# Kernel optimization log

Hardware: AMD Instinct MI355X
Metric: run time of the kernel (lower is better)

The kernel has to match this reference:

```python
import jax, jax.numpy as jnp
import numpy as np

B, C, H, W = 512, 1, 280, 280
KS, S, P_PAD, F = 28, 28, 0, 16
HS = (H - KS + 2 * P_PAD) // S + 1  # 10
WS = (W - KS + 2 * P_PAD) // S + 1  # 10
P = HS * WS                          # 100 patches
OUT = 10


def setup_inputs() -> dict:
    key = jax.random.key(0)
    k1, k2, k3, k4, k5 = jax.random.split(key, 5)
    x = jax.random.normal(k1, (B, C, H, W), dtype=jnp.float32)
    weight = jax.random.normal(k2, (P * F, C, KS, KS), dtype=jnp.float32) * 0.05
    bias = jax.random.normal(k3, (P * F, C), dtype=jnp.float32) * 0.05
    dec_w = jax.random.normal(k4, (OUT, P * F * C), dtype=jnp.float32) * 0.05
    dec_b = jax.random.normal(k5, (OUT,), dtype=jnp.float32) * 0.05
    return {"x": x, "weight": weight, "bias": bias, "dec_w": dec_w, "dec_b": dec_b}


def _extract_patches(x):
    # x: (B, C, H+2p, W+2p) -> (B, P, C, KS, KS), patch order: row-major over (hs, ws)
    rows = jnp.arange(HS)[:, None] * S + jnp.arange(KS)[None, :]  # (HS, KS)
    cols = jnp.arange(WS)[:, None] * S + jnp.arange(KS)[None, :]  # (WS, KS)
    p = x[:, :, rows, :]            # (B, C, HS, KS, W)
    p = p[:, :, :, :, cols]         # (B, C, HS, KS, WS, KS)
    p = p.transpose(0, 2, 4, 1, 3, 5)  # (B, HS, WS, C, KS, KS)
    return p.reshape(B, P, C, KS, KS)


def reference(x, weight, bias, dec_w, dec_b):
    xp = jnp.pad(x, ((0, 0), (0, 0), (P_PAD, P_PAD), (P_PAD, P_PAD)))
    patches = _extract_patches(xp)                       # (B, P, C, KS, KS)
    # torch: x.repeat(1, f, ...) tiles patches f times; weight flat index i -> (f_idx, p_idx)
    w = weight.reshape(F, P, C, KS, KS)
    y = jnp.einsum('bpckl,fpckl->bfpc', patches, w)      # (B, F, P, C)
    y = y + bias.reshape(F, P, C)
    y = jax.nn.relu(y)
    y = y.reshape(B, F * P * C)
    return y @ dec_w.T + dec_b
```

## Files before the change

### kernel.cpp

```cpp
#include <hip/hip_runtime.h>
#include <stdint.h>

#define BATCH 512
#define HWIMG 78400
#define WROW  280
#define KSZ   28
#define PNUM  100
#define FNUM  16
#define ONUM  10

#define BT    64
#define CH    7
#define XF4   (BT * 28)
#define WF4   (FNUM * 28)

typedef __attribute__((address_space(1))) const void cg_void;
typedef __attribute__((address_space(3))) void lds_void;

__global__ __launch_bounds__(256) void init_out(const float* __restrict__ dec_b,
                                                float* __restrict__ out) {
    int i = blockIdx.x * 256 + threadIdx.x;
    if (i < BATCH * ONUM) out[i] = dec_b[i % ONUM];
}

__global__ __launch_bounds__(256) void lcn_fused(
    const float* __restrict__ x,
    const float* __restrict__ weight,
    const float* __restrict__ bias,
    const float* __restrict__ dec_w,
    float* __restrict__ out)
{
    __shared__ float4 lx[2][XF4];
    __shared__ float4 lw[2][WF4];

    const int t  = threadIdx.x;
    const int kg = t & 7;
    const int fg = (t >> 3) & 3;
    const int bg = t >> 5;
    const int bx = blockIdx.x;
    const int p  = bx >> 3;
    const int bt = bx & 7;
    const int pr = p / 10, pc = p % 10;
    const int b0 = bt * BT;

    const float* xs[7];
#pragma unroll
    for (int s = 0; s < 7; ++s) {
        int idx = s * 256 + t;
        int b  = idx / 28, rf = idx % 28;
        int r0 = rf / 7,   c4 = rf % 7;
        xs[s] = x + (size_t)(b0 + b) * HWIMG + (size_t)(pr * 28 + r0) * WROW
                  + pc * 28 + c4 * 4;
    }
    const int wi1 = 256 + (t < 192 ? t : t - 64);
    const float* ws0;
    const float* ws1;
    {
        int f = t / 28, rf = t % 28;
        ws0 = weight + ((size_t)(f * PNUM + p)) * 784 + rf * 4;
        f = wi1 / 28; rf = wi1 % 28;
        ws1 = weight + ((size_t)(f * PNUM + p)) * 784 + rf * 4;
    }

    auto issue_chunk = [&](int cc, int bb) {
#pragma unroll
        for (int s = 0; s < 7; ++s)
            __builtin_amdgcn_global_load_lds((cg_void*)(xs[s] + (size_t)cc * 4 * WROW),
                                             (lds_void*)&lx[bb][s * 256 + t], 16, 0, 0);
        __builtin_amdgcn_global_load_lds((cg_void*)(ws0 + (size_t)cc * 112),
                                         (lds_void*)&lw[bb][t], 16, 0, 0);
        __builtin_amdgcn_global_load_lds((cg_void*)(ws1 + (size_t)cc * 112),
                                         (lds_void*)&lw[bb][wi1], 16, 0, 0);
    };

    issue_chunk(0, 0);
    issue_chunk(1, 1);

    float acc[8][4];
#pragma unroll
    for (int i = 0; i < 8; ++i)
#pragma unroll
        for (int j = 0; j < 4; ++j) acc[i][j] = 0.f;

    const int kge = (kg < 7) ? kg : 0;

#pragma unroll
    for (int c = 0; c < CH; ++c) {
        const int buf = c & 1;
        if (c < CH - 1) asm volatile("s_waitcnt vmcnt(9)" ::: "memory");
        else            asm volatile("s_waitcnt vmcnt(0)" ::: "memory");
        __builtin_amdgcn_s_barrier();
        asm volatile("" ::: "memory");

#pragma unroll
        for (int m = 0; m < 4; ++m) {
            float4 wv[4];
#pragma unroll
            for (int j = 0; j < 4; ++j)
                wv[j] = lw[buf][(fg * 4 + j) * 28 + m * 7 + kge];
#pragma unroll
            for (int i = 0; i < 8; ++i) {
                float4 av = lx[buf][(bg * 8 + i) * 28 + m * 7 + kge];
#pragma unroll
                for (int j = 0; j < 4; ++j) {
                    acc[i][j] = fmaf(av.x, wv[j].x, acc[i][j]);
                    acc[i][j] = fmaf(av.y, wv[j].y, acc[i][j]);
                    acc[i][j] = fmaf(av.z, wv[j].z, acc[i][j]);
                    acc[i][j] = fmaf(av.w, wv[j].w, acc[i][j]);
                }
            }
        }

        asm volatile("" ::: "memory");
        __builtin_amdgcn_s_barrier();
        if (c + 2 < CH) issue_chunk(c + 2, buf);
    }

    const float km = (kg < 7) ? 1.f : 0.f;
#pragma unroll
    for (int i = 0; i < 8; ++i)
#pragma unroll
        for (int j = 0; j < 4; ++j) acc[i][j] *= km;

#pragma unroll
    for (int d = 1; d < 8; d <<= 1)
#pragma unroll
        for (int i = 0; i < 8; ++i)
#pragma unroll
            for (int j = 0; j < 4; ++j)
                acc[i][j] += __shfl_xor(acc[i][j], d, 64);

    float y[8][4];
#pragma unroll
    for (int j = 0; j < 4; ++j) {
        const float bs = bias[(fg * 4 + j) * PNUM + p];
#pragma unroll
        for (int i = 0; i < 8; ++i) {
            float v = acc[i][j] + bs;
            y[i][j] = v > 0.f ? v : 0.f;
        }
    }

    float po[8][2];
    const int  o0  = kg * 2;
    const bool act = (kg < 5);
    if (act) {
        float dwv[4][2];
#pragma unroll
        for (int j = 0; j < 4; ++j)
#pragma unroll
            for (int oo = 0; oo < 2; ++oo)
                dwv[j][oo] = dec_w[(size_t)(o0 + oo) * (PNUM * FNUM) + (fg * 4 + j) * PNUM + p];
#pragma unroll
        for (int i = 0; i < 8; ++i)
#pragma unroll
            for (int oo = 0; oo < 2; ++oo) {
                float s = 0.f;
#pragma unroll
                for (int j = 0; j < 4; ++j) s = fmaf(y[i][j], dwv[j][oo], s);
                po[i][oo] = s;
            }
    } else {
#pragma unroll
        for (int i = 0; i < 8; ++i) { po[i][0] = 0.f; po[i][1] = 0.f; }
    }

#pragma unroll
    for (int d = 8; d < 32; d <<= 1)
#pragma unroll
        for (int i = 0; i < 8; ++i)
#pragma unroll
            for (int oo = 0; oo < 2; ++oo)
                po[i][oo] += __shfl_xor(po[i][oo], d, 64);

    if (act && fg == 0) {
#pragma unroll
        for (int i = 0; i < 8; ++i)
#pragma unroll
            for (int oo = 0; oo < 2; ++oo)
                atomicAdd(&out[(size_t)(b0 + bg * 8 + i) * ONUM + o0 + oo], po[i][oo]);
    }
}

extern "C" void kernel_launch(void* const* d_in, const int* in_sizes, int n_in,
                              void* d_out, int out_size, void* d_ws, size_t ws_size,
                              hipStream_t stream) {
    const float* x     = (const float*)d_in[0];
    const float* w     = (const float*)d_in[1];
    const float* bias  = (const float*)d_in[2];
    const float* dec_w = (const float*)d_in[3];
    const float* dec_b = (const float*)d_in[4];
    float* out = (float*)d_out;

    init_out<<<(BATCH * ONUM + 255) / 256, 256, 0, stream>>>(dec_b, out);
    lcn_fused<<<(BATCH / BT) * PNUM, 256, 0, stream>>>(x, w, bias, dec_w, out);
}
```

Measured before the change: 256.3 us.

## Retile LCN kernel to 2-row chunks, 4x8 thread tiles, padded LDS stride

The K dimension is now split into 14 two-row chunks instead of 7 four-row chunks, which shrinks the LDS double buffers, and the kernel requests 4 blocks per CU through launch bounds. The per-thread tile changes from 8 batches by 4 filters to 4 batches by 8 filters, and the x tile uses a padded row stride of 15 float4 to reduce LDS bank conflicts. The aim is higher occupancy and better latency hiding. The cost is twice as many barrier and wait rounds, plus an added lgkmcnt wait before each buffer refill.

```diff
diff --git a/kernel.cpp b/kernel.cpp
--- a/kernel.cpp
+++ b/kernel.cpp
@@ -10,9 +10,10 @@
 #define ONUM  10
 
 #define BT    64
-#define CH    7
-#define XF4   (BT * 28)
-#define WF4   (FNUM * 28)
+#define NCH   14
+#define XSTR  15
+#define XF4   1024
+#define WF4   256
 
 typedef __attribute__((address_space(1))) const void cg_void;
 typedef __attribute__((address_space(3))) void lds_void;
@@ -23,7 +24,7 @@
     if (i < BATCH * ONUM) out[i] = dec_b[i % ONUM];
 }
 
-__global__ __launch_bounds__(256) void lcn_fused(
+__global__ __launch_bounds__(256, 4) void lcn_fused(
     const float* __restrict__ x,
     const float* __restrict__ weight,
     const float* __restrict__ bias,
@@ -35,74 +36,70 @@
 
     const int t  = threadIdx.x;
     const int kg = t & 7;
-    const int fg = (t >> 3) & 3;
-    const int bg = t >> 5;
+    const int fg = (t >> 3) & 1;
+    const int bg = t >> 4;
     const int bx = blockIdx.x;
     const int p  = bx >> 3;
     const int bt = bx & 7;
     const int pr = p / 10, pc = p % 10;
     const int b0 = bt * BT;
 
-    const float* xs[7];
+    const float* xsrc[4];
 #pragma unroll
-    for (int s = 0; s < 7; ++s) {
-        int idx = s * 256 + t;
-        int b  = idx / 28, rf = idx % 28;
-        int r0 = rf / 7,   c4 = rf % 7;
-        xs[s] = x + (size_t)(b0 + b) * HWIMG + (size_t)(pr * 28 + r0) * WROW
-                  + pc * 28 + c4 * 4;
+    for (int s = 0; s < 4; ++s) {
+        int slot = s * 256 + t;
+        int b = slot / XSTR, rf = slot % XSTR;
+        if (slot >= 960 || rf >= 14) { b = 0; rf = 0; }
+        int r = rf / 7, c4 = rf % 7;
+        xsrc[s] = x + (size_t)(b0 + b) * HWIMG + (size_t)(pr * 28 + r) * WROW + pc * 28 + c4 * 4;
     }
-    const int wi1 = 256 + (t < 192 ? t : t - 64);
-    const float* ws0;
-    const float* ws1;
+    const float* wsrc;
     {
-        int f = t / 28, rf = t % 28;
-        ws0 = weight + ((size_t)(f * PNUM + p)) * 784 + rf * 4;
-        f = wi1 / 28; rf = wi1 % 28;
-        ws1 = weight + ((size_t)(f * PNUM + p)) * 784 + rf * 4;
+        int slot = (t < 224) ? t : 0;
+        int f = slot / 14, rf = slot % 14;
+        int r = rf / 7, c4 = rf % 7;
+        wsrc = weight + (size_t)(f * PNUM + p) * 784 + r * KSZ + c4 * 4;
     }
 
     auto issue_chunk = [&](int cc, int bb) {
 #pragma unroll
-        for (int s = 0; s < 7; ++s)
-            __builtin_amdgcn_global_load_lds((cg_void*)(xs[s] + (size_t)cc * 4 * WROW),
+        for (int s = 0; s < 4; ++s)
+            __builtin_amdgcn_global_load_lds((cg_void*)(xsrc[s] + (size_t)cc * 2 * WROW),
                                              (lds_void*)&lx[bb][s * 256 + t], 16, 0, 0);
-        __builtin_amdgcn_global_load_lds((cg_void*)(ws0 + (size_t)cc * 112),
+        __builtin_amdgcn_global_load_lds((cg_void*)(wsrc + (size_t)cc * 2 * KSZ),
                                          (lds_void*)&lw[bb][t], 16, 0, 0);
-        __builtin_amdgcn_global_load_lds((cg_void*)(ws1 + (size_t)cc * 112),
-                                         (lds_void*)&lw[bb][wi1], 16, 0, 0);
     };
 
     issue_chunk(0, 0);
     issue_chunk(1, 1);
 
-    float acc[8][4];
+    float acc[4][8];
 #pragma unroll
-    for (int i = 0; i < 8; ++i)
+    for (int i = 0; i < 4; ++i)
 #pragma unroll
-        for (int j = 0; j < 4; ++j) acc[i][j] = 0.f;
+        for (int j = 0; j < 8; ++j) acc[i][j] = 0.f;
 
     const int kge = (kg < 7) ? kg : 0;
 
 #pragma unroll
-    for (int c = 0; c < CH; ++c) {
+    for (int c = 0; c < NCH; ++c) {
         const int buf = c & 1;
-        if (c < CH - 1) asm volatile("s_waitcnt vmcnt(9)" ::: "memory");
-        else            asm volatile("s_waitcnt vmcnt(0)" ::: "memory");
+        if (c < NCH - 1) asm volatile("s_waitcnt vmcnt(5)" ::: "memory");
+        else             asm volatile("s_waitcnt vmcnt(0)" ::: "memory");
         __builtin_amdgcn_s_barrier();
         asm volatile("" ::: "memory");
 
 #pragma unroll
-        for (int m = 0; m < 4; ++m) {
-            float4 wv[4];
+        for (int r = 0; r < 2; ++r) {
+            float4 wv[8];
 #pragma unroll
-            for (int j = 0; j < 4; ++j)
-                wv[j] = lw[buf][(fg * 4 + j) * 28 + m * 7 + kge];
+            for (int j = 0; j < 8; ++j)
+                wv[j] = lw[buf][(fg * 8 + j) * 14 + r * 7 + kge];
 #pragma unroll
-            for (int i = 0; i < 8; ++i) {
-                float4 av = lx[buf][(bg * 8 + i) * 28 + m * 7 + kge];
+            for (int i = 0; i < 4; ++i) {
+                float4 av = lx[buf][(bg * 4 + i) * XSTR + r * 7 + kge];
 #pragma unroll
-                for (int j = 0; j < 4; ++j) {
+                for (int j = 0; j < 8; ++j) {
                     acc[i][j] = fmaf(av.x, wv[j].x, acc[i][j]);
                     acc[i][j] = fmaf(av.y, wv[j].y, acc[i][j]);
                     acc[i][j] = fmaf(av.z, wv[j].z, acc[i][j]);
@@ -111,74 +108,73 @@
             }
         }
 
+        asm volatile("s_waitcnt lgkmcnt(0)" ::: "memory");
+        __builtin_amdgcn_s_barrier();
         asm volatile("" ::: "memory");
-        __builtin_amdgcn_s_barrier();
-        if (c + 2 < CH) issue_chunk(c + 2, buf);
+        if (c + 2 < NCH) issue_chunk(c + 2, buf);
     }
 
     const float km = (kg < 7) ? 1.f : 0.f;
 #pragma unroll
-    for (int i = 0; i < 8; ++i)
+    for (int i = 0; i < 4; ++i)
 #pragma unroll
-        for (int j = 0; j < 4; ++j) acc[i][j] *= km;
+        for (int j = 0; j < 8; ++j) acc[i][j] *= km;
 
 #pragma unroll
     for (int d = 1; d < 8; d <<= 1)
 #pragma unroll
-        for (int i = 0; i < 8; ++i)
+        for (int i = 0; i < 4; ++i)
 #pragma unroll
-            for (int j = 0; j < 4; ++j)
+            for (int j = 0; j < 8; ++j)
                 acc[i][j] += __shfl_xor(acc[i][j], d, 64);
 
-    float y[8][4];
+    float y[4][8];
 #pragma unroll
-    for (int j = 0; j < 4; ++j) {
-        const float bs = bias[(fg * 4 + j) * PNUM + p];
+    for (int j = 0; j < 8; ++j) {
+        const float bs = bias[(fg * 8 + j) * PNUM + p];
 #pragma unroll
-        for (int i = 0; i < 8; ++i) {
+        for (int i = 0; i < 4; ++i) {
             float v = acc[i][j] + bs;
             y[i][j] = v > 0.f ? v : 0.f;
         }
     }
 
-    float po[8][2];
+    float po[4][2];
     const int  o0  = kg * 2;
     const bool act = (kg < 5);
     if (act) {
-        float dwv[4][2];
+        float dwv[8][2];
 #pragma unroll
-        for (int j = 0; j < 4; ++j)
+        for (int j = 0; j < 8; ++j)
 #pragma unroll
             for (int oo = 0; oo < 2; ++oo)
-                dwv[j][oo] = dec_w[(size_t)(o0 + oo) * (PNUM * FNUM) + (fg * 4 + j) * PNUM + p];
+                dwv[j][oo] = dec_w[(size_t)(o0 + oo) * (PNUM * FNUM) + (fg * 8 + j) * PNUM + p];
 #pragma unroll
-        for (int i = 0; i < 8; ++i)
+        for (int i = 0; i < 4; ++i)
 #pragma unroll
             for (int oo = 0; oo < 2; ++oo) {
                 float s = 0.f;
 #pragma unroll
-                for (int j = 0; j < 4; ++j) s = fmaf(y[i][j], dwv[j][oo], s);
+                for (int j = 0; j < 8; ++j) s = fmaf(y[i][j], dwv[j][oo], s);
                 po[i][oo] = s;
             }
     } else {
 #pragma unroll
-        for (int i = 0; i < 8; ++i) { po[i][0] = 0.f; po[i][1] = 0.f; }
+        for (int i = 0; i < 4; ++i) { po[i][0] = 0.f; po[i][1] = 0.f; }
     }
 
 #pragma unroll
-    for (int d = 8; d < 32; d <<= 1)
+    for (int i = 0; i < 4; ++i)
 #pragma unroll
-        for (int i = 0; i < 8; ++i)
-#pragma unroll
-            for (int oo = 0; oo < 2; ++oo)
-                po[i][oo] += __shfl_xor(po[i][oo], d, 64);
+        for (int oo = 0; oo < 2; ++oo)
+            po[i][oo] += __shfl_xor(po[i][oo], 8, 64);
 
     if (act && fg == 0) {
 #pragma unroll
-        for (int i = 0; i < 8; ++i)
+        for (int i = 0; i < 4; ++i)
 #pragma unroll
             for (int oo = 0; oo < 2; ++oo)
-                atomicAdd(&out[(size_t)(b0 + bg * 8 + i) * ONUM + o0 + oo], po[i][oo]);
+                atomicAdd(&out[(size_t)(b0 + bg * 4 + i) * ONUM + o0 + oo], po[i][oo]);
     }
 }
 
```

Result: slower. 302.2 us (+17.9%).

## Halve K-chunk to two rows with odd LDS stride to cut bank conflicts

Applied to the files above, without the earlier changes.

Each pipeline chunk now covers 2 image rows instead of 4, so there are 14 chunks instead of 7. Shared-memory rows are padded to an odd float4 stride of 15, which is meant to reduce LDS bank conflicts on the float4 reads, and fewer loads are issued per thread per chunk. The main loop is unrolled by 2 instead of fully, and the waitcnt value is changed to match. In exchange there are twice as many barriers and waits, with less work between them to hide memory latency.

```diff
diff --git a/kernel.cpp b/kernel.cpp
--- a/kernel.cpp
+++ b/kernel.cpp
@@ -10,9 +10,11 @@
 #define ONUM  10
 
 #define BT    64
-#define CH    7
-#define XF4   (BT * 28)
-#define WF4   (FNUM * 28)
+#define NCH   14
+#define XSTR  15
+#define WSTR  15
+#define XF4   1024
+#define WF4   256
 
 typedef __attribute__((address_space(1))) const void cg_void;
 typedef __attribute__((address_space(3))) void lds_void;
@@ -43,34 +45,30 @@
     const int pr = p / 10, pc = p % 10;
     const int b0 = bt * BT;
 
-    const float* xs[7];
+    const float* xsrc[4];
 #pragma unroll
-    for (int s = 0; s < 7; ++s) {
-        int idx = s * 256 + t;
-        int b  = idx / 28, rf = idx % 28;
-        int r0 = rf / 7,   c4 = rf % 7;
-        xs[s] = x + (size_t)(b0 + b) * HWIMG + (size_t)(pr * 28 + r0) * WROW
-                  + pc * 28 + c4 * 4;
+    for (int s = 0; s < 4; ++s) {
+        int slot = s * 256 + t;
+        int b = slot / XSTR, rf = slot % XSTR;
+        if (b >= BT || rf >= 14) { b = 0; rf = 0; }
+        int r = rf / 7, c4 = rf % 7;
+        xsrc[s] = x + (size_t)(b0 + b) * HWIMG + (size_t)(pr * 28 + r) * WROW + pc * 28 + c4 * 4;
     }
-    const int wi1 = 256 + (t < 192 ? t : t - 64);
-    const float* ws0;
-    const float* ws1;
+    const float* wsrc;
     {
-        int f = t / 28, rf = t % 28;
-        ws0 = weight + ((size_t)(f * PNUM + p)) * 784 + rf * 4;
-        f = wi1 / 28; rf = wi1 % 28;
-        ws1 = weight + ((size_t)(f * PNUM + p)) * 784 + rf * 4;
+        int f = t / WSTR, rf = t % WSTR;
+        if (f >= FNUM || rf >= 14) { f = 0; rf = 0; }
+        int r = rf / 7, c4 = rf % 7;
+        wsrc = weight + (size_t)(f * PNUM + p) * 784 + r * KSZ + c4 * 4;
     }
 
     auto issue_chunk = [&](int cc, int bb) {
 #pragma unroll
-        for (int s = 0; s < 7; ++s)
-            __builtin_amdgcn_global_load_lds((cg_void*)(xs[s] + (size_t)cc * 4 * WROW),
+        for (int s = 0; s < 4; ++s)
+            __builtin_amdgcn_global_load_lds((cg_void*)(xsrc[s] + (size_t)cc * 2 * WROW),
                                              (lds_void*)&lx[bb][s * 256 + t], 16, 0, 0);
-        __builtin_amdgcn_global_load_lds((cg_void*)(ws0 + (size_t)cc * 112),
+        __builtin_amdgcn_global_load_lds((cg_void*)(wsrc + (size_t)cc * 2 * KSZ),
                                          (lds_void*)&lw[bb][t], 16, 0, 0);
-        __builtin_amdgcn_global_load_lds((cg_void*)(ws1 + (size_t)cc * 112),
-                                         (lds_void*)&lw[bb][wi1], 16, 0, 0);
     };
 
     issue_chunk(0, 0);
@@ -84,23 +82,23 @@
 
     const int kge = (kg < 7) ? kg : 0;
 
-#pragma unroll
-    for (int c = 0; c < CH; ++c) {
+#pragma unroll 2
+    for (int c = 0; c < NCH; ++c) {
         const int buf = c & 1;
-        if (c < CH - 1) asm volatile("s_waitcnt vmcnt(9)" ::: "memory");
-        else            asm volatile("s_waitcnt vmcnt(0)" ::: "memory");
+        if (c + 1 < NCH) asm volatile("s_waitcnt vmcnt(5)" ::: "memory");
+        else             asm volatile("s_waitcnt vmcnt(0)" ::: "memory");
         __builtin_amdgcn_s_barrier();
         asm volatile("" ::: "memory");
 
 #pragma unroll
-        for (int m = 0; m < 4; ++m) {
+        for (int r = 0; r < 2; ++r) {
             float4 wv[4];
 #pragma unroll
             for (int j = 0; j < 4; ++j)
-                wv[j] = lw[buf][(fg * 4 + j) * 28 + m * 7 + kge];
+                wv[j] = lw[buf][(fg * 4 + j) * WSTR + r * 7 + kge];
 #pragma unroll
             for (int i = 0; i < 8; ++i) {
-                float4 av = lx[buf][(bg * 8 + i) * 28 + m * 7 + kge];
+                float4 av = lx[buf][(bg * 8 + i) * XSTR + r * 7 + kge];
 #pragma unroll
                 for (int j = 0; j < 4; ++j) {
                     acc[i][j] = fmaf(av.x, wv[j].x, acc[i][j]);
@@ -113,7 +111,8 @@
 
         asm volatile("" ::: "memory");
         __builtin_amdgcn_s_barrier();
-        if (c + 2 < CH) issue_chunk(c + 2, buf);
+        asm volatile("" ::: "memory");
+        if (c + 2 < NCH) issue_chunk(c + 2, buf);
     }
 
     const float km = (kg < 7) ? 1.f : 0.f;
```

Result: slower. 275.3 us (+7.4%).
